# Kernel tuning notes

Measured on AMD Instinct MI355X. Metric: run time of the kernel, lower is better.

Reference implementation:

```python
import jax, jax.numpy as jnp
import numpy as np

B, L, D, H, FF = 2, 2048, 1024, 16, 4096
DH = D // H
EPS = 1e-5  # torch LayerNorm default


def _layernorm(x, g, b):
    mu = jnp.mean(x, axis=-1, keepdims=True)
    var = jnp.mean(jnp.square(x - mu), axis=-1, keepdims=True)
    return (x - mu) * jax.lax.rsqrt(var + EPS) * g + b


def setup_inputs() -> dict:
    key = jax.random.key(0)
    ks = jax.random.split(key, 8)
    s = 0.02  # typical init scale for weights
    return {
        "x": jax.random.normal(ks[0], (B, L, D), jnp.float32),
        "pos_embed": jax.random.normal(ks[1], (1, L, D), jnp.float32) * s,
        "ln1_g": jnp.ones((D,), jnp.float32),
        "ln1_b": jnp.zeros((D,), jnp.float32),
        "Wq": jax.random.normal(ks[2], (D, D), jnp.float32) * s,
        "Wk": jax.random.normal(ks[3], (D, D), jnp.float32) * s,
        "Wv": jax.random.normal(ks[4], (D, D), jnp.float32) * s,
        "Wo": jax.random.normal(ks[5], (D, D), jnp.float32) * s,
        "bo": jnp.zeros((D,), jnp.float32),
        "ln2_g": jnp.ones((D,), jnp.float32),
        "ln2_b": jnp.zeros((D,), jnp.float32),
        "W1": jax.random.normal(ks[6], (D, FF), jnp.float32) * s,
        "b1": jnp.zeros((FF,), jnp.float32),
        "W2": jax.random.normal(ks[7], (FF, D), jnp.float32) * s,
        "b2": jnp.zeros((D,), jnp.float32),
    }


def reference(x, pos_embed, ln1_g, ln1_b, Wq, Wk, Wv, Wo, bo, ln2_g, ln2_b, W1, b1, W2, b2):
    scale = DH ** -0.5
    residual = x
    h = _layernorm(x, ln1_g, ln1_b) + pos_embed  # [B,L,D]
    # qkv projections (no bias, qkv_bias=False default), split into heads
    q = (h @ Wq).reshape(B, L, H, DH).transpose(0, 2, 1, 3)  # [B,H,L,DH]
    k = (h @ Wk).reshape(B, L, H, DH).transpose(0, 2, 1, 3)
    v = (h @ Wv).reshape(B, L, H, DH).transpose(0, 2, 1, 3)
    attn = jnp.einsum("bhqd,bhkd->bhqk", q, k) * scale  # [B,H,L,L]
    attn = jax.nn.softmax(attn, axis=-1)
    out = jnp.einsum("bhqk,bhkd->bhqd", attn, v)  # [B,H,L,DH]
    out = out.transpose(0, 2, 1, 3).reshape(B, L, D)
    out = out @ Wo + bo
    x = residual + out
    # MLP with pre-norm
    m = _layernorm(x, ln2_g, ln2_b)
    m = jax.nn.gelu(m @ W1 + b1, approximate=False) @ W2 + b2
    return x + m
```

## Files before the change

### kernel.cpp

```cpp
#include <hip/hip_runtime.h>
#include <hip/hip_bf16.h>
#include <cstdint>

typedef __bf16 bf16_t;
typedef __bf16 bf16x8 __attribute__((ext_vector_type(8)));
typedef __bf16 bf16x4v __attribute__((ext_vector_type(4)));
typedef short s16x4 __attribute__((ext_vector_type(4)));
typedef float f32x4 __attribute__((ext_vector_type(4)));

#define B_ 2
#define L_ 2048
#define D_ 1024
#define H_ 16
#define DH_ 64
#define FF_ 4096
#define M_TOT (B_*L_)

#define CLOG2 0.18033688011112042f


__device__ __forceinline__ void gload_lds16(const void* g, void* l) {
    __builtin_amdgcn_global_load_lds((__attribute__((address_space(1))) void*)g,
                                     (__attribute__((address_space(3))) void*)l,
                                     16, 0, 0);
}

__device__ __forceinline__ float fast_exp2(float v) {
    return __builtin_amdgcn_exp2f(v);
}

__device__ __forceinline__ float gelu_fast(float x) {
    float x3 = x * x * x;
    float y  = fmaf(0.044715f, x3, x);
    float e  = fast_exp2(y * 2.3022213f);
    float t  = fmaf(-2.0f, __builtin_amdgcn_rcpf(e + 1.0f), 1.0f);
    return 0.5f * x * (1.0f + t);
}

__global__ void transpose_bf16_kernel(const float* __restrict__ W, bf16_t* __restrict__ WT,
                                      int K, int N) {
    __shared__ float t[32][33];
    int tx = threadIdx.x, ty = threadIdx.y;
    int n0 = blockIdx.x * 32, k0 = blockIdx.y * 32;
#pragma unroll
    for (int i = 0; i < 4; i++)
        t[ty + 8 * i][tx] = W[(size_t)(k0 + ty + 8 * i) * N + n0 + tx];
    __syncthreads();
#pragma unroll
    for (int i = 0; i < 4; i++)
        WT[(size_t)(n0 + ty + 8 * i) * K + k0 + tx] = (bf16_t)t[tx][ty + 8 * i];
}

__global__ void transpose_qkvo_kernel(const float* __restrict__ Wq, const float* __restrict__ Wk,
                                      const float* __restrict__ Wv, const float* __restrict__ Wo,
                                      bf16_t* __restrict__ WqkvT, bf16_t* __restrict__ WoT) {
    int z = blockIdx.z;
    const float* W = (z == 0) ? Wq : (z == 1) ? Wk : (z == 2) ? Wv : Wo;
    bf16_t* dst = (z < 3) ? (WqkvT + (size_t)z * 1024 * 1024) : WoT;
    __shared__ float t[32][33];
    int tx = threadIdx.x, ty = threadIdx.y;
    int n0 = blockIdx.x * 32, k0 = blockIdx.y * 32;
#pragma unroll
    for (int i = 0; i < 4; i++)
        t[ty + 8 * i][tx] = W[(size_t)(k0 + ty + 8 * i) * D_ + n0 + tx];
    __syncthreads();
#pragma unroll
    for (int i = 0; i < 4; i++)
        dst[(size_t)(n0 + ty + 8 * i) * D_ + k0 + tx] = (bf16_t)t[tx][ty + 8 * i];
}

__global__ __launch_bounds__(256) void ln_kernel(const float* __restrict__ x,
                                                 const float* __restrict__ pos,
                                                 const float* __restrict__ g,
                                                 const float* __restrict__ beta,
                                                 bf16_t* __restrict__ out) {
    int row = blockIdx.x, tid = threadIdx.x;
    const float* xr = x + (size_t)row * D_;
    float v[4];
    float s = 0.f, sq = 0.f;
#pragma unroll
    for (int i = 0; i < 4; i++) {
        float a = xr[tid + 256 * i];
        v[i] = a; s += a; sq += a * a;
    }
#pragma unroll
    for (int o = 32; o > 0; o >>= 1) { s += __shfl_xor(s, o); sq += __shfl_xor(sq, o); }
    __shared__ float red[8];
    int wid = tid >> 6;
    if ((tid & 63) == 0) { red[wid] = s; red[4 + wid] = sq; }
    __syncthreads();
    s  = red[0] + red[1] + red[2] + red[3];
    sq = red[4] + red[5] + red[6] + red[7];
    float mu  = s * (1.f / D_);
    float var = sq * (1.f / D_) - mu * mu;
    float rs  = rsqrtf(var + 1e-5f);
    int l = row & (L_ - 1);
#pragma unroll
    for (int i = 0; i < 4; i++) {
        int c = tid + 256 * i;
        float hv = (v[i] - mu) * rs * g[c] + beta[c];
        if (pos) hv += pos[(size_t)l * D_ + c];
        out[(size_t)row * D_ + c] = (bf16_t)hv;
    }
}

__global__ __launch_bounds__(256) void ln_fuse_kernel(const float* __restrict__ x,
                                                      const float* __restrict__ bo,
                                                      const float* __restrict__ P0,
                                                      const float* __restrict__ P1,
                                                      const float* __restrict__ g,
                                                      const float* __restrict__ beta,
                                                      float* __restrict__ x2,
                                                      bf16_t* __restrict__ out) {
    int row = blockIdx.x, tid = threadIdx.x;
    size_t base = (size_t)row * D_;
    float v[4];
    float s = 0.f, sq = 0.f;
#pragma unroll
    for (int i = 0; i < 4; i++) {
        int c = tid + 256 * i;
        float a = x[base + c] + bo[c] + P0[base + c] + P1[base + c];
        v[i] = a; s += a; sq += a * a;
        x2[base + c] = a;
    }
#pragma unroll
    for (int o = 32; o > 0; o >>= 1) { s += __shfl_xor(s, o); sq += __shfl_xor(sq, o); }
    __shared__ float red[8];
    int wid = tid >> 6;
    if ((tid & 63) == 0) { red[wid] = s; red[4 + wid] = sq; }
    __syncthreads();
    s  = red[0] + red[1] + red[2] + red[3];
    sq = red[4] + red[5] + red[6] + red[7];
    float mu  = s * (1.f / D_);
    float var = sq * (1.f / D_) - mu * mu;
    float rs  = rsqrtf(var + 1e-5f);
#pragma unroll
    for (int i = 0; i < 4; i++) {
        int c = tid + 256 * i;
        out[base + c] = (bf16_t)((v[i] - mu) * rs * g[c] + beta[c]);
    }
}

__global__ __launch_bounds__(256) void reduce_out_kernel(const float* __restrict__ x2,
                                                         const float* __restrict__ bias,
                                                         const float* __restrict__ P1,
                                                         float* __restrict__ dout) {
    int i = (blockIdx.x * 256 + threadIdx.x) * 4;
    float4 a  = *(const float4*)(x2 + i);
    float4 bv = *(const float4*)(bias + (i & (D_ - 1)));
    float4 p0 = *(const float4*)(dout + i);
    float4 p1 = *(const float4*)(P1 + i);
    a.x += bv.x + p0.x + p1.x;
    a.y += bv.y + p0.y + p1.y;
    a.z += bv.z + p0.z + p1.z;
    a.w += bv.w + p0.w + p1.w;
    *(float4*)(dout + i) = a;
}

template <int EPI, typename OutT>
__global__ __launch_bounds__(256) void gemm_kernel(const bf16_t* __restrict__ A,
                                                   const bf16_t* __restrict__ BT,
                                                   OutT* __restrict__ C,
                                                   const float* __restrict__ bias,
                                                   bf16_t* __restrict__ Vt,
                                                   int M, int N, int K) {
    __shared__ __align__(16) bf16_t sA[2][128 * 32];
    __shared__ __align__(16) bf16_t sB[2][128 * 32];
    int tid = threadIdx.x;
    int lane = tid & 63, w = tid >> 6, wy = w >> 1, wx = w & 1;
    int qm = lane & 15, quad = lane >> 4;
    int row0 = blockIdx.x * 128, col0 = blockIdx.y * 128;
    f32x4 acc[4][4] = {};
    int sf[2], sra[2], scol[2];
#pragma unroll
    for (int c = 0; c < 2; c++) {
        int f = tid * 8 + c * 2048;
        sf[c] = f;
        sra[c] = f >> 5;
        int ch = (f >> 3) & 3;
        scol[c] = ((ch ^ ((sra[c] >> 1) & 3)) << 3);
    }
    int aoff[4], boff[4];
#pragma unroll
    for (int t = 0; t < 4; t++) {
        int Ra = wy * 64 + t * 16 + qm;
        int Rb = wx * 64 + t * 16 + qm;
        aoff[t] = Ra * 32 + ((quad ^ ((Ra >> 1) & 3)) << 3);
        boff[t] = Rb * 32 + ((quad ^ ((Rb >> 1) & 3)) << 3);
    }
    const bf16_t* Ab = A  + (size_t)row0 * K;
    const bf16_t* Bb = BT + (size_t)col0 * K;
#pragma unroll
    for (int c = 0; c < 2; c++) {
        gload_lds16(Ab + (size_t)sra[c] * K + scol[c], &sA[0][sf[c]]);
        gload_lds16(Bb + (size_t)sra[c] * K + scol[c], &sB[0][sf[c]]);
    }
    for (int k0 = 0; k0 < K; k0 += 32) {
        int cur = (k0 >> 5) & 1;
        __syncthreads();
        int kn = k0 + 32;
        if (kn < K) {
#pragma unroll
            for (int c = 0; c < 2; c++) {
                gload_lds16(Ab + (size_t)sra[c] * K + kn + scol[c], &sA[cur ^ 1][sf[c]]);
                gload_lds16(Bb + (size_t)sra[c] * K + kn + scol[c], &sB[cur ^ 1][sf[c]]);
            }
        }
        bf16x8 af[4], bfr[4];
#pragma unroll
        for (int mt = 0; mt < 4; mt++) af[mt] = *(const bf16x8*)&sA[cur][aoff[mt]];
#pragma unroll
        for (int nt = 0; nt < 4; nt++) bfr[nt] = *(const bf16x8*)&sB[cur][boff[nt]];
#pragma unroll
        for (int mt = 0; mt < 4; mt++)
#pragma unroll
            for (int nt = 0; nt < 4; nt++)
                acc[mt][nt] = __builtin_amdgcn_mfma_f32_16x16x32_bf16(af[mt], bfr[nt],
                                                                      acc[mt][nt], 0, 0, 0);
    }
    if (EPI == 4 && col0 >= 2048) {
#pragma unroll
        for (int mt = 0; mt < 4; mt++) {
            int row_base = row0 + wy * 64 + mt * 16 + quad * 4;
            int bb = row_base >> 11, key0 = row_base & 2047;
#pragma unroll
            for (int nt = 0; nt < 4; nt++) {
                int vcol = col0 - 2048 + wx * 64 + nt * 16 + qm;
                int hh = vcol >> 6, dd = vcol & 63;
                bf16x4v pk;
#pragma unroll
                for (int r = 0; r < 4; r++) pk[r] = (bf16_t)acc[mt][nt][r];
                *(bf16x4v*)&Vt[(size_t)(((bb << 4) + hh) * 64 + dd) * 2048 + key0] = pk;
            }
        }
        return;
    }
    float qscale = (EPI == 4 && col0 < 1024) ? CLOG2 : 1.0f;
#pragma unroll
    for (int mt = 0; mt < 4; mt++) {
#pragma unroll
        for (int nt = 0; nt < 4; nt++) {
            int col = col0 + wx * 64 + nt * 16 + qm;
#pragma unroll
            for (int r = 0; r < 4; r++) {
                int row = row0 + wy * 64 + mt * 16 + quad * 4 + r;
                float v = acc[mt][nt][r];
                if (EPI == 2) { v += bias[col]; v = gelu_fast(v); }
                if (EPI == 4) C[(size_t)row * 2048 + col] = (OutT)(v * qscale);
                else          C[(size_t)row * N + col] = (OutT)v;
            }
        }
    }
}

__global__ __launch_bounds__(256) void gemm_splitk_st_kernel(const bf16_t* __restrict__ A,
                                                             const bf16_t* __restrict__ BT,
                                                             float* __restrict__ P0,
                                                             float* __restrict__ P1,
                                                             int N, int Ktot, int Ksplit) {
    __shared__ __align__(16) bf16_t sA[2][128 * 32];
    __shared__ __align__(16) bf16_t sB[2][128 * 32];
    int tid = threadIdx.x;
    int lane = tid & 63, w = tid >> 6, wy = w >> 1, wx = w & 1;
    int qm = lane & 15, quad = lane >> 4;
    int row0 = blockIdx.x * 128, col0 = blockIdx.y * 128;
    size_t koff = (size_t)blockIdx.z * Ksplit;
    f32x4 acc[4][4] = {};
    int sf[2], sra[2], scol[2];
#pragma unroll
    for (int c = 0; c < 2; c++) {
        int f = tid * 8 + c * 2048;
        sf[c] = f;
        sra[c] = f >> 5;
        int ch = (f >> 3) & 3;
        scol[c] = ((ch ^ ((sra[c] >> 1) & 3)) << 3);
    }
    int aoff[4], boff[4];
#pragma unroll
    for (int t = 0; t < 4; t++) {
        int Ra = wy * 64 + t * 16 + qm;
        int Rb = wx * 64 + t * 16 + qm;
        aoff[t] = Ra * 32 + ((quad ^ ((Ra >> 1) & 3)) << 3);
        boff[t] = Rb * 32 + ((quad ^ ((Rb >> 1) & 3)) << 3);
    }
    const bf16_t* Ab = A  + (size_t)row0 * Ktot + koff;
    const bf16_t* Bb = BT + (size_t)col0 * Ktot + koff;
#pragma unroll
    for (int c = 0; c < 2; c++) {
        gload_lds16(Ab + (size_t)sra[c] * Ktot + scol[c], &sA[0][sf[c]]);
        gload_lds16(Bb + (size_t)sra[c] * Ktot + scol[c], &sB[0][sf[c]]);
    }
    for (int k0 = 0; k0 < Ksplit; k0 += 32) {
        int cur = (k0 >> 5) & 1;
        __syncthreads();
        int kn = k0 + 32;
        if (kn < Ksplit) {
#pragma unroll
            for (int c = 0; c < 2; c++) {
                gload_lds16(Ab + (size_t)sra[c] * Ktot + kn + scol[c], &sA[cur ^ 1][sf[c]]);
                gload_lds16(Bb + (size_t)sra[c] * Ktot + kn + scol[c], &sB[cur ^ 1][sf[c]]);
            }
        }
        bf16x8 af[4], bfr[4];
#pragma unroll
        for (int mt = 0; mt < 4; mt++) af[mt] = *(const bf16x8*)&sA[cur][aoff[mt]];
#pragma unroll
        for (int nt = 0; nt < 4; nt++) bfr[nt] = *(const bf16x8*)&sB[cur][boff[nt]];
#pragma unroll
        for (int mt = 0; mt < 4; mt++)
#pragma unroll
            for (int nt = 0; nt < 4; nt++)
                acc[mt][nt] = __builtin_amdgcn_mfma_f32_16x16x32_bf16(af[mt], bfr[nt],
                                                                      acc[mt][nt], 0, 0, 0);
    }
    float* P = blockIdx.z ? P1 : P0;
#pragma unroll
    for (int mt = 0; mt < 4; mt++) {
#pragma unroll
        for (int nt = 0; nt < 4; nt++) {
            int col = col0 + wx * 64 + nt * 16 + qm;
#pragma unroll
            for (int r = 0; r < 4; r++) {
                int row = row0 + wy * 64 + mt * 16 + quad * 4 + r;
                P[(size_t)row * N + col] = acc[mt][nt][r];
            }
        }
    }
}

__global__ __launch_bounds__(256) void attn_kernel(const bf16_t* __restrict__ QK,
                                                   const bf16_t* __restrict__ Vt,
                                                   bf16_t* __restrict__ O) {
    __shared__ __align__(16) bf16_t sK[2][64 * 64];
    __shared__ __align__(16) bf16_t sV[2][64 * 64];
    int tid = threadIdx.x, lane = tid & 63, w = tid >> 6;
    int qm = lane & 15, quad = lane >> 4;
    int q0 = blockIdx.x * 128 + w * 32;
    int bh = blockIdx.y, b = bh >> 4, h = bh & 15;

    const bf16_t* Qbase = QK + (size_t)(b * L_) * 2048 + h * 64;
    const bf16_t* Kbase = Qbase + 1024;
    const bf16_t* Vbase = Vt + (size_t)bh * 64 * 2048;

    bf16x8 qf[2][2];
#pragma unroll
    for (int g = 0; g < 2; g++) {
        const bf16_t* qp = Qbase + (size_t)(q0 + g * 16 + qm) * 2048 + quad * 8;
        qf[g][0] = *(const bf16x8*)qp;
        qf[g][1] = *(const bf16x8*)(qp + 32);
    }

    int f0 = tid * 8, f1 = f0 + 2048;
    int r0 = f0 >> 6, sc0 = ((((f0 >> 3) & 7) ^ (r0 & 7)) << 3);
    int r1 = f1 >> 6, sc1 = ((((f1 >> 3) & 7) ^ (r1 & 7)) << 3);

    gload_lds16(Kbase + (size_t)r0 * 2048 + sc0, &sK[0][f0]);
    gload_lds16(Kbase + (size_t)r1 * 2048 + sc1, &sK[0][f1]);
    gload_lds16(Vbase + (size_t)r0 * 2048 + sc0, &sV[0][f0]);
    gload_lds16(Vbase + (size_t)r1 * 2048 + sc1, &sV[0][f1]);

    f32x4 o[2][4] = {};
    float l_[2] = {0.f, 0.f};

    int kfo[4][2], vfo[4][4];
#pragma unroll
    for (int kt = 0; kt < 4; kt++) {
#pragma unroll
        for (int ks = 0; ks < 2; ks++) {
            int row = kt * 16 + qm;
            kfo[kt][ks] = row * 64 + ((((ks << 2) + quad) ^ (row & 7)) << 3);
        }
#pragma unroll
        for (int dt = 0; dt < 4; dt++) {
            int row = dt * 16 + qm;
            int cw = (kt << 1) + (quad >> 1);
            vfo[dt][kt] = row * 64 + ((cw ^ (row & 7)) << 3) + ((quad & 1) << 2);
        }
    }

    for (int kv0 = 0; kv0 < L_; kv0 += 64) {
        int cur = (kv0 >> 6) & 1;
        __syncthreads();
        int kn = kv0 + 64;
        if (kn < L_) {
            gload_lds16(Kbase + (size_t)(kn + r0) * 2048 + sc0, &sK[cur ^ 1][f0]);
            gload_lds16(Kbase + (size_t)(kn + r1) * 2048 + sc1, &sK[cur ^ 1][f1]);
            gload_lds16(Vbase + (size_t)r0 * 2048 + kn + sc0, &sV[cur ^ 1][f0]);
            gload_lds16(Vbase + (size_t)r1 * 2048 + kn + sc1, &sV[cur ^ 1][f1]);
        }

        bf16x8 kf[4][2];
#pragma unroll
        for (int kt = 0; kt < 4; kt++)
#pragma unroll
            for (int ks = 0; ks < 2; ks++)
                kf[kt][ks] = *(const bf16x8*)&sK[cur][kfo[kt][ks]];
        f32x4 s[2][4] = {};
#pragma unroll
        for (int kt = 0; kt < 4; kt++)
#pragma unroll
            for (int ks = 0; ks < 2; ks++) {
                s[0][kt] = __builtin_amdgcn_mfma_f32_16x16x32_bf16(kf[kt][ks], qf[0][ks], s[0][kt], 0, 0, 0);
                s[1][kt] = __builtin_amdgcn_mfma_f32_16x16x32_bf16(kf[kt][ks], qf[1][ks], s[1][kt], 0, 0, 0);
            }

        s16x4 pf[2][4];
#pragma unroll
        for (int g = 0; g < 2; g++) {
            float sum = l_[g];
#pragma unroll
            for (int kt = 0; kt < 4; kt++) {
                union { bf16x4v b; s16x4 i; } u;
#pragma unroll
                for (int r = 0; r < 4; r++) {
                    float p = fast_exp2(s[g][kt][r]);
                    sum += p;
                    u.b[r] = (bf16_t)p;
                }
                pf[g][kt] = u.i;
            }
            l_[g] = sum;
        }

#pragma unroll
        for (int dt = 0; dt < 4; dt++)
#pragma unroll
            for (int kt = 0; kt < 4; kt++) {
                s16x4 vf = *(const s16x4*)&sV[cur][vfo[dt][kt]];
                o[0][dt] = __builtin_amdgcn_mfma_f32_16x16x16bf16_1k(vf, pf[0][kt], o[0][dt], 0, 0, 0);
                o[1][dt] = __builtin_amdgcn_mfma_f32_16x16x16bf16_1k(vf, pf[1][kt], o[1][dt], 0, 0, 0);
            }
    }

#pragma unroll
    for (int g = 0; g < 2; g++) {
        float lt = l_[g];
        lt += __shfl_xor(lt, 16);
        lt += __shfl_xor(lt, 32);
        float rl = 1.0f / lt;
        size_t row = (size_t)(b * L_ + q0 + g * 16 + qm);
#pragma unroll
        for (int dt = 0; dt < 4; dt++) {
            bf16x4v pk;
#pragma unroll
            for (int r = 0; r < 4; r++) pk[r] = (bf16_t)(o[g][dt][r] * rl);
            *(bf16x4v*)&O[row * D_ + h * 64 + dt * 16 + quad * 4] = pk;
        }
    }
}


extern "C" void kernel_launch(void* const* d_in, const int* in_sizes, int n_in,
                              void* d_out, int out_size, void* d_ws, size_t ws_size,
                              hipStream_t stream) {
    const float* x   = (const float*)d_in[0];
    const float* pos = (const float*)d_in[1];
    const float* g1  = (const float*)d_in[2];
    const float* be1 = (const float*)d_in[3];
    const float* Wq  = (const float*)d_in[4];
    const float* Wk  = (const float*)d_in[5];
    const float* Wv  = (const float*)d_in[6];
    const float* Wo  = (const float*)d_in[7];
    const float* bo  = (const float*)d_in[8];
    const float* g2  = (const float*)d_in[9];
    const float* be2 = (const float*)d_in[10];
    const float* W1  = (const float*)d_in[11];
    const float* b1m = (const float*)d_in[12];
    const float* W2  = (const float*)d_in[13];
    const float* b2m = (const float*)d_in[14];

    char* ws = (char*)d_ws;
    const size_t MB = 1ull << 20;
    bf16_t* W2T   = (bf16_t*)(ws + 0);
    float*  x2    = (float*) (ws + 8 * MB);
    bf16_t* qk    = (bf16_t*)(ws + 24 * MB);
    bf16_t* Vt    = (bf16_t*)(ws + 40 * MB);
    bf16_t* hb    = (bf16_t*)(ws + 48 * MB);
    float*  Pwo0  = (float*) (ws + 24 * MB);
    float*  Pwo1  = (float*) (ws + 40 * MB);
    bf16_t* attnO = (bf16_t*)(ws + 56 * MB);
    bf16_t* mb    = (bf16_t*)(ws + 56 * MB);
    bf16_t* ff1   = (bf16_t*)(ws + 24 * MB);
    bf16_t* W1T   = (bf16_t*)(ws + 64 * MB);
    float*  Pff1  = (float*) (ws + 56 * MB);
    bf16_t* WqkvT = (bf16_t*)(ws + 72 * MB);
    bf16_t* WoT   = (bf16_t*)(ws + 78 * MB);

    dim3 tb(32, 8);
    transpose_qkvo_kernel<<<dim3(32, 32, 4), tb, 0, stream>>>(Wq, Wk, Wv, Wo, WqkvT, WoT);
    transpose_bf16_kernel<<<dim3(128, 32), tb, 0, stream>>>(W1, W1T, D_, FF_);
    transpose_bf16_kernel<<<dim3(32, 128), tb, 0, stream>>>(W2, W2T, FF_, D_);

    ln_kernel<<<M_TOT, 256, 0, stream>>>(x, pos, g1, be1, hb);

    gemm_kernel<4, bf16_t><<<dim3(32, 24), 256, 0, stream>>>(hb, WqkvT, qk, nullptr,
                                                             Vt, M_TOT, 3072, D_);

    attn_kernel<<<dim3(16, 32), 256, 0, stream>>>(qk, Vt, attnO);

    gemm_splitk_st_kernel<<<dim3(32, 8, 2), 256, 0, stream>>>(attnO, WoT, Pwo0, Pwo1,
                                                              D_, D_, D_ / 2);

    ln_fuse_kernel<<<M_TOT, 256, 0, stream>>>(x, bo, Pwo0, Pwo1, g2, be2, x2, mb);

    gemm_kernel<2, bf16_t><<<dim3(32, 32), 256, 0, stream>>>(mb, W1T, ff1, b1m,
                                                             nullptr, M_TOT, FF_, D_);

    gemm_splitk_st_kernel<<<dim3(32, 8, 2), 256, 0, stream>>>(ff1, W2T, (float*)d_out,
                                                              Pff1, D_, FF_, FF_ / 2);

    reduce_out_kernel<<<M_TOT * D_ / 1024, 256, 0, stream>>>(x2, b2m, Pff1, (float*)d_out);

    (void)in_sizes; (void)n_in; (void)out_size; (void)ws_size;
}
```

Before: 370.6 us.

## Give each attention wave 64 query rows with 128-thread blocks

The attention kernel now launches 2 waves per block instead of 4, and each wave handles 64 query rows (4 groups of 16) instead of 32. Each K and V fragment read from LDS is reused across four MFMA groups, halving the per-block LDS read traffic per query, and each thread now issues four async loads per tile instead of two. The cost is more accumulator and score registers per wave (o[4][4], s[4][4], pf[4][4]), which may lower occupancy, and fewer waves are left to hide latency inside each block.

Result: slower. 394.0 us (+6.3%).

```diff
diff --git a/kernel.cpp b/kernel.cpp
--- a/kernel.cpp
+++ b/kernel.cpp
@@ -328,39 +328,44 @@
     }
 }
 
-__global__ __launch_bounds__(256) void attn_kernel(const bf16_t* __restrict__ QK,
-                                                   const bf16_t* __restrict__ Vt,
-                                                   bf16_t* __restrict__ O) {
+__global__ __launch_bounds__(128, 2) void attn_kernel(const bf16_t* __restrict__ QK,
+                                                      const bf16_t* __restrict__ Vt,
+                                                      bf16_t* __restrict__ O) {
     __shared__ __align__(16) bf16_t sK[2][64 * 64];
     __shared__ __align__(16) bf16_t sV[2][64 * 64];
     int tid = threadIdx.x, lane = tid & 63, w = tid >> 6;
     int qm = lane & 15, quad = lane >> 4;
-    int q0 = blockIdx.x * 128 + w * 32;
+    int q0 = blockIdx.x * 128 + w * 64;
     int bh = blockIdx.y, b = bh >> 4, h = bh & 15;
 
     const bf16_t* Qbase = QK + (size_t)(b * L_) * 2048 + h * 64;
     const bf16_t* Kbase = Qbase + 1024;
     const bf16_t* Vbase = Vt + (size_t)bh * 64 * 2048;
 
-    bf16x8 qf[2][2];
-#pragma unroll
-    for (int g = 0; g < 2; g++) {
+    bf16x8 qf[4][2];
+#pragma unroll
+    for (int g = 0; g < 4; g++) {
         const bf16_t* qp = Qbase + (size_t)(q0 + g * 16 + qm) * 2048 + quad * 8;
         qf[g][0] = *(const bf16x8*)qp;
         qf[g][1] = *(const bf16x8*)(qp + 32);
     }
 
-    int f0 = tid * 8, f1 = f0 + 2048;
-    int r0 = f0 >> 6, sc0 = ((((f0 >> 3) & 7) ^ (r0 & 7)) << 3);
-    int r1 = f1 >> 6, sc1 = ((((f1 >> 3) & 7) ^ (r1 & 7)) << 3);
-
-    gload_lds16(Kbase + (size_t)r0 * 2048 + sc0, &sK[0][f0]);
-    gload_lds16(Kbase + (size_t)r1 * 2048 + sc1, &sK[0][f1]);
-    gload_lds16(Vbase + (size_t)r0 * 2048 + sc0, &sV[0][f0]);
-    gload_lds16(Vbase + (size_t)r1 * 2048 + sc1, &sV[0][f1]);
-
-    f32x4 o[2][4] = {};
-    float l_[2] = {0.f, 0.f};
+    int sf[4], sr[4], scc[4];
+#pragma unroll
+    for (int c = 0; c < 4; c++) {
+        int f = tid * 8 + c * 1024;
+        sf[c] = f;
+        sr[c] = f >> 6;
+        scc[c] = ((((f >> 3) & 7) ^ (sr[c] & 7)) << 3);
+    }
+#pragma unroll
+    for (int c = 0; c < 4; c++) {
+        gload_lds16(Kbase + (size_t)sr[c] * 2048 + scc[c], &sK[0][sf[c]]);
+        gload_lds16(Vbase + (size_t)sr[c] * 2048 + scc[c], &sV[0][sf[c]]);
+    }
+
+    f32x4 o[4][4] = {};
+    float l_[4] = {0.f, 0.f, 0.f, 0.f};
 
     int kfo[4][2], vfo[4][4];
 #pragma unroll
@@ -383,30 +388,28 @@
         __syncthreads();
         int kn = kv0 + 64;
         if (kn < L_) {
-            gload_lds16(Kbase + (size_t)(kn + r0) * 2048 + sc0, &sK[cur ^ 1][f0]);
-            gload_lds16(Kbase + (size_t)(kn + r1) * 2048 + sc1, &sK[cur ^ 1][f1]);
-            gload_lds16(Vbase + (size_t)r0 * 2048 + kn + sc0, &sV[cur ^ 1][f0]);
-            gload_lds16(Vbase + (size_t)r1 * 2048 + kn + sc1, &sV[cur ^ 1][f1]);
-        }
-
-        bf16x8 kf[4][2];
-#pragma unroll
-        for (int kt = 0; kt < 4; kt++)
-#pragma unroll
-            for (int ks = 0; ks < 2; ks++)
-                kf[kt][ks] = *(const bf16x8*)&sK[cur][kfo[kt][ks]];
-        f32x4 s[2][4] = {};
-#pragma unroll
-        for (int kt = 0; kt < 4; kt++)
+#pragma unroll
+            for (int c = 0; c < 4; c++) {
+                gload_lds16(Kbase + (size_t)(kn + sr[c]) * 2048 + scc[c], &sK[cur ^ 1][sf[c]]);
+                gload_lds16(Vbase + (size_t)sr[c] * 2048 + kn + scc[c], &sV[cur ^ 1][sf[c]]);
+            }
+        }
+
+        f32x4 s[4][4] = {};
+#pragma unroll
+        for (int kt = 0; kt < 4; kt++) {
 #pragma unroll
             for (int ks = 0; ks < 2; ks++) {
-                s[0][kt] = __builtin_amdgcn_mfma_f32_16x16x32_bf16(kf[kt][ks], qf[0][ks], s[0][kt], 0, 0, 0);
-                s[1][kt] = __builtin_amdgcn_mfma_f32_16x16x32_bf16(kf[kt][ks], qf[1][ks], s[1][kt], 0, 0, 0);
-            }
-
-        s16x4 pf[2][4];
-#pragma unroll
-        for (int g = 0; g < 2; g++) {
+                bf16x8 kf = *(const bf16x8*)&sK[cur][kfo[kt][ks]];
+#pragma unroll
+                for (int g = 0; g < 4; g++)
+                    s[g][kt] = __builtin_amdgcn_mfma_f32_16x16x32_bf16(kf, qf[g][ks], s[g][kt], 0, 0, 0);
+            }
+        }
+
+        s16x4 pf[4][4];
+#pragma unroll
+        for (int g = 0; g < 4; g++) {
             float sum = l_[g];
 #pragma unroll
             for (int kt = 0; kt < 4; kt++) {
@@ -427,13 +430,14 @@
 #pragma unroll
             for (int kt = 0; kt < 4; kt++) {
                 s16x4 vf = *(const s16x4*)&sV[cur][vfo[dt][kt]];
-                o[0][dt] = __builtin_amdgcn_mfma_f32_16x16x16bf16_1k(vf, pf[0][kt], o[0][dt], 0, 0, 0);
-                o[1][dt] = __builtin_amdgcn_mfma_f32_16x16x16bf16_1k(vf, pf[1][kt], o[1][dt], 0, 0, 0);
-            }
-    }
-
-#pragma unroll
-    for (int g = 0; g < 2; g++) {
+#pragma unroll
+                for (int g = 0; g < 4; g++)
+                    o[g][dt] = __builtin_amdgcn_mfma_f32_16x16x16bf16_1k(vf, pf[g][kt], o[g][dt], 0, 0, 0);
+            }
+    }
+
+#pragma unroll
+    for (int g = 0; g < 4; g++) {
         float lt = l_[g];
         lt += __shfl_xor(lt, 16);
         lt += __shfl_xor(lt, 32);
@@ -496,7 +500,7 @@
     gemm_kernel<4, bf16_t><<<dim3(32, 24), 256, 0, stream>>>(hb, WqkvT, qk, nullptr,
                                                              Vt, M_TOT, 3072, D_);
 
-    attn_kernel<<<dim3(16, 32), 256, 0, stream>>>(qk, Vt, attnO);
+    attn_kernel<<<dim3(16, 32), 128, 0, stream>>>(qk, Vt, attnO);
 
     gemm_splitk_st_kernel<<<dim3(32, 8, 2), 256, 0, stream>>>(attnO, WoT, Pwo0, Pwo1,
                                                               D_, D_, D_ / 2);
```
